# Kernel tuning notes

Measured on AMD Instinct MI355X. Metric: run time of the kernel, lower is better.

## Reference

```python
import jax, jax.numpy as jnp
import numpy as np

B, N, M, F, BF = 16, 1024, 12, 64, 128
N_CONV = 3
VOCAB = 100
BN_EPS = 1e-3  # keras BatchNormalization default epsilon


def _bn(x, gamma, beta):
    # inference-mode BN with moving_mean=0, moving_var=1 (keras defaults)
    return gamma * (x * (1.0 / jnp.sqrt(1.0 + BN_EPS))) + beta


def setup_inputs() -> dict:
    key = jax.random.key(0)
    ks = jax.random.split(key, 16)
    in_fea = 2 * F + BF
    inp = {
        'atom_types': jax.random.randint(ks[0], (B, N), 0, VOCAB, dtype=jnp.int32),
        'bond_fea': jax.random.normal(ks[1], (B, N, M, BF), dtype=jnp.float32),
        'nbr_list': jax.random.randint(ks[2], (B, N, M), 0, N, dtype=jnp.int32),
        'target_index': jax.random.randint(ks[3], (B, 64), 0, N, dtype=jnp.int32),
        'emb': jax.random.normal(ks[4], (VOCAB, F), dtype=jnp.float32) * 0.05,
        'core_w': jax.random.normal(ks[5], (N_CONV, in_fea, F), dtype=jnp.float32) / np.sqrt(in_fea),
        'core_b': jnp.zeros((N_CONV, F), dtype=jnp.float32),
        'filt_w': jax.random.normal(ks[6], (N_CONV, in_fea, 1), dtype=jnp.float32) / np.sqrt(in_fea),
        'filt_b': jnp.zeros((N_CONV, 1), dtype=jnp.float32),
        'bna_g': jnp.ones((N_CONV, F), dtype=jnp.float32),
        'bna_b': jnp.zeros((N_CONV, F), dtype=jnp.float32),
        'bnb_g': jnp.ones((N_CONV, F), dtype=jnp.float32),
        'bnb_b': jnp.zeros((N_CONV, F), dtype=jnp.float32),
        'dense_w': jax.random.normal(ks[7], (F, F), dtype=jnp.float32) / np.sqrt(F),
        'dense_b': jnp.zeros((F,), dtype=jnp.float32),
    }
    return inp


def _cgcnn_layer(x, bond_fea, nbr_list, cw, cb, fw, fb, bag, bab, bbg, bbb):
    # x: (B,N,F); bond_fea: (B,N,M,BF); nbr_list: (B,N,M)
    bidx = jnp.arange(x.shape[0])[:, None, None]
    atom_nbr = x[bidx, nbr_list]                       # (B,N,M,F) gather_nd
    atom_self = jnp.broadcast_to(x[:, :, None, :], atom_nbr.shape)
    total = jnp.concatenate([atom_self, atom_nbr, bond_fea], axis=-1)  # (B,N,M,2F+BF)
    core = total @ cw + cb                             # (B,N,M,F)
    filt = total @ fw + fb                             # (B,N,M,1)
    core = _bn(core, bag, bab)
    filt = jax.nn.softmax(filt, axis=2)                # softmax over neighbors
    core = jax.nn.relu(core)
    summed = jnp.mean(filt * core, axis=2)             # (B,N,F)
    summed = _bn(summed, bbg, bbb)
    return jax.nn.relu(x + summed)


def reference(atom_types, bond_fea, nbr_list, target_index, emb, core_w, core_b,
              filt_w, filt_b, bna_g, bna_b, bnb_g, bnb_b, dense_w, dense_b):
    x = emb[atom_types]                                # (B,N,F)
    for l in range(N_CONV):
        x = _cgcnn_layer(x, bond_fea, nbr_list, core_w[l], core_b[l],
                         filt_w[l], filt_b[l], bna_g[l], bna_b[l], bnb_g[l], bnb_b[l])
    bidx = jnp.arange(x.shape[0])[:, None]
    crys = x[bidx, target_index]                       # (B,N0,F) pooling gather
    crys = jax.nn.relu(crys)
    out = jax.nn.relu(crys @ dense_w + dense_b)        # (B,N0,F)
    return out
```

## Files before the change

### kernel.cpp

```cpp
#include <hip/hip_runtime.h>
#include <hip/hip_bf16.h>


#define BB 16
#define NN 1024
#define MM 12
#define FF 64
#define BFE 128
#define RT (BB * NN * MM)
#define S_BN 0.99950037f
#define WCOLS 208
#define WSTR 136

typedef __attribute__((ext_vector_type(8))) short bf16x8;
typedef __attribute__((ext_vector_type(4))) float f32x4;

static __device__ __forceinline__ unsigned short f2bf(float f) {
    union { float f; unsigned u; } c; c.f = f;
    unsigned r = c.u + 0x7fff + ((c.u >> 16) & 1);
    return (unsigned short)(r >> 16);
}
static __device__ __forceinline__ float bf2f(unsigned short s) {
    union { unsigned u; float f; } c; c.u = ((unsigned)s) << 16;
    return c.f;
}

__global__ void fold_w(const float* __restrict__ cw, const float* __restrict__ cb,
                       const float* __restrict__ g,  const float* __restrict__ bab,
                       float* __restrict__ cwp, float* __restrict__ cbp) {
    int i = blockIdx.x * 256 + threadIdx.x;
    if (i >= 3 * 256 * 64) return;
    int f = i & 63;
    int l = i / (256 * 64);
    float gs = g[l * 64 + f] * S_BN;
    cwp[i] = cw[i] * gs;
    if (((i >> 6) & 255) == 0)
        cbp[l * 64 + f] = cb[l * 64 + f] * gs + bab[l * 64 + f];
}

__global__ void prep_wT(const float* __restrict__ cw, const float* __restrict__ g,
                        const float* __restrict__ fw, unsigned short* __restrict__ wT) {
    int i = blockIdx.x * 256 + threadIdx.x;
    if (i >= WCOLS * WSTR) return;
    int col = i / WSTR, k = i % WSTR;
    float v = 0.f;
    if (k < 128) {
        if (col < 192) {
            int l = col >> 6, f = col & 63;
            v = cw[(l * 256 + 128 + k) * 64 + f] * g[l * 64 + f] * S_BN;
        } else if (col < 195) {
            int l = col - 192;
            v = fw[l * 256 + 128 + k];
        }
    }
    wT[i] = f2bf(v);
}

__global__ void embed_k(const int* __restrict__ at, const float* __restrict__ emb,
                        float* __restrict__ x) {
    int i = blockIdx.x * 256 + threadIdx.x;
    int f = i & 63;
    int bn = i >> 6;
    x[i] = emb[at[bn] * FF + f];
}

__global__ __launch_bounds__(256) void gemm_bond(
    const float* __restrict__ bond, const unsigned short* __restrict__ wT,
    unsigned short* __restrict__ core, float* __restrict__ filt) {
    __shared__ unsigned short bsh[WCOLS * WSTR];
    __shared__ unsigned short ash[64 * WSTR];
    int tid = threadIdx.x;
    int w = tid >> 6, lane = tid & 63;
    int row0 = blockIdx.x * 64;

    const float4* wsrc = (const float4*)wT;
    float4* wdst = (float4*)bsh;
    #pragma unroll
    for (int i = 0; i < 14; i++) {
        int idx = tid + 256 * i;
        if (idx < (WCOLS * WSTR * 2) / 16) wdst[idx] = wsrc[idx];
    }
    const float4* bsrc = (const float4*)(bond + (size_t)row0 * BFE);
    #pragma unroll
    for (int i = 0; i < 8; i++) {
        int idx = tid + 256 * i;
        float4 v = bsrc[idx];
        int r = idx >> 5, c4 = idx & 31;
        ushort4 h;
        h.x = f2bf(v.x); h.y = f2bf(v.y); h.z = f2bf(v.z); h.w = f2bf(v.w);
        *(ushort4*)&ash[r * WSTR + c4 * 4] = h;
    }
    __syncthreads();

    int m = lane & 15, quad = lane >> 4;
    f32x4 acc[13];
    #pragma unroll
    for (int t = 0; t < 13; t++) acc[t] = (f32x4){0.f, 0.f, 0.f, 0.f};

    #pragma unroll
    for (int c = 0; c < 4; c++) {
        bf16x8 af = *(const bf16x8*)&ash[(w * 16 + m) * WSTR + c * 32 + quad * 8];
        #pragma unroll
        for (int t = 0; t < 13; t++) {
            bf16x8 bfv = *(const bf16x8*)&bsh[(t * 16 + m) * WSTR + c * 32 + quad * 8];
            acc[t] = __builtin_amdgcn_mfma_f32_16x16x32_bf16(af, bfv, acc[t], 0, 0, 0);
        }
    }

    int rbase = row0 + w * 16 + quad * 4;
    #pragma unroll
    for (int t = 0; t < 12; t++) {
        int l = t >> 2;
        int f = (t & 3) * 16 + m;
        #pragma unroll
        for (int r = 0; r < 4; r++)
            core[((size_t)l * RT + rbase + r) * 64 + f] = f2bf(acc[t][r]);
    }
    if (m < 3) {
        #pragma unroll
        for (int r = 0; r < 4; r++)
            filt[(size_t)m * RT + rbase + r] = acc[12][r];
    }
}

__global__ __launch_bounds__(256) void atomproj(
    const float* __restrict__ x, const float* __restrict__ cwp_l,
    const float* __restrict__ cbp_l, const float* __restrict__ fw_l,
    const float* __restrict__ fb_l,
    float* __restrict__ ys, float* __restrict__ yn,
    float* __restrict__ fs, float* __restrict__ fn) {
    __shared__ float wsh[128 * 64];
    __shared__ float xs[4][64];
    int tid = threadIdx.x, w = tid >> 6, lane = tid & 63;
    #pragma unroll
    for (int i = 0; i < 8; i++)
        ((float4*)wsh)[tid + 256 * i] = ((const float4*)cwp_l)[tid + 256 * i];
    float fw1 = fw_l[lane], fw2 = fw_l[64 + lane];
    float cb = cbp_l[lane], fbv = fb_l[0];
    __syncthreads();
    #pragma unroll 1
    for (int it = 0; it < 4; it++) {
        int row = (blockIdx.x * 4 + it) * 4 + w;
        float xl = x[(size_t)row * 64 + lane];
        xs[w][lane] = xl;
        float a1 = cb, a2 = 0.f;
        #pragma unroll 16
        for (int k = 0; k < 64; k++) {
            float xv = xs[w][k];
            a1 += xv * wsh[k * 64 + lane];
            a2 += xv * wsh[(64 + k) * 64 + lane];
        }
        ys[(size_t)row * 64 + lane] = a1;
        yn[(size_t)row * 64 + lane] = a2;
        float p1 = xl * fw1, p2 = xl * fw2;
        #pragma unroll
        for (int off = 32; off; off >>= 1) {
            p1 += __shfl_xor(p1, off, 64);
            p2 += __shfl_xor(p2, off, 64);
        }
        if (lane == 0) { fs[row] = p1 + fbv; fn[row] = p2; }
    }
}

__global__ __launch_bounds__(256) void layer_ep(
    const float* __restrict__ x, const unsigned short* __restrict__ core_l,
    const float* __restrict__ filt_l, const int* __restrict__ nbr,
    const float* __restrict__ ys, const float* __restrict__ yn,
    const float* __restrict__ fs, const float* __restrict__ fn,
    const float* __restrict__ bbg, const float* __restrict__ bbb,
    float* __restrict__ xout) {
    int tid = threadIdx.x, w = tid >> 6, lane = tid & 63;
    int row = blockIdx.x * 4 + w;
    int base = (row >> 10) * NN;
    size_t rb = (size_t)row * MM;

    int jv[MM]; float fltv[MM], corev[MM];
    #pragma unroll
    for (int mm = 0; mm < MM; mm++) jv[mm] = nbr[rb + mm];
    float fsv = fs[row], ysv = ys[(size_t)row * 64 + lane];
    #pragma unroll
    for (int mm = 0; mm < MM; mm++)
        fltv[mm] = filt_l[rb + mm] + fsv + fn[base + jv[mm]];
    #pragma unroll
    for (int mm = 0; mm < MM; mm++)
        corev[mm] = bf2f(core_l[(rb + mm) * 64 + lane]) + ysv
                  + yn[(size_t)(base + jv[mm]) * 64 + lane];
    float fmax = -1e30f;
    #pragma unroll
    for (int mm = 0; mm < MM; mm++) fmax = fmaxf(fmax, fltv[mm]);
    float fsum = 0.f;
    #pragma unroll
    for (int mm = 0; mm < MM; mm++) { fltv[mm] = __expf(fltv[mm] - fmax); fsum += fltv[mm]; }
    float inv = 1.f / (12.f * fsum);
    float summed = 0.f;
    #pragma unroll
    for (int mm = 0; mm < MM; mm++) summed += fltv[mm] * fmaxf(corev[mm], 0.f);
    summed *= inv;
    float o = x[(size_t)row * 64 + lane] + bbg[lane] * (summed * S_BN) + bbb[lane];
    xout[(size_t)row * 64 + lane] = fmaxf(o, 0.f);
}

__global__ __launch_bounds__(256) void final_k(
    const float* __restrict__ x, const int* __restrict__ tidx,
    const float* __restrict__ dw, const float* __restrict__ db,
    float* __restrict__ out) {
    __shared__ float xs[4][64];
    __shared__ float wsh[64 * 64];
    int tid = threadIdx.x;
    int w = tid >> 6, lane = tid & 63;
    const float4* src = (const float4*)dw;
    float4* dst = (float4*)wsh;
    #pragma unroll
    for (int i = 0; i < 4; i++) dst[tid + 256 * i] = src[tid + 256 * i];
    int row = blockIdx.x * 4 + w;
    int b = row >> 6;
    int t = tidx[row];
    float xv = x[((size_t)b * NN + t) * 64 + lane];
    xs[w][lane] = fmaxf(xv, 0.f);
    __syncthreads();
    float a = db[lane];
    #pragma unroll 16
    for (int k = 0; k < 64; k++) a += xs[w][k] * wsh[k * 64 + lane];
    out[row * 64 + lane] = fmaxf(a, 0.f);
}

extern "C" void kernel_launch(void* const* d_in, const int* in_sizes, int n_in,
                              void* d_out, int out_size, void* d_ws, size_t ws_size,
                              hipStream_t stream) {
    const int*   at   = (const int*)d_in[0];
    const float* bond = (const float*)d_in[1];
    const int*   nbr  = (const int*)d_in[2];
    const int*   tgt  = (const int*)d_in[3];
    const float* emb  = (const float*)d_in[4];
    const float* cw   = (const float*)d_in[5];
    const float* cb   = (const float*)d_in[6];
    const float* fw   = (const float*)d_in[7];
    const float* fb   = (const float*)d_in[8];
    const float* bag  = (const float*)d_in[9];
    const float* bab  = (const float*)d_in[10];
    const float* bbg  = (const float*)d_in[11];
    const float* bbb  = (const float*)d_in[12];
    const float* dw   = (const float*)d_in[13];
    const float* db   = (const float*)d_in[14];

    float* ws   = (float*)d_ws;
    float* xA   = ws;
    float* xB   = xA + (size_t)BB * NN * FF;
    float* cwp  = xB + (size_t)BB * NN * FF;
    float* cbp  = cwp + 3 * 256 * 64;
    float* ys   = cbp + 192;
    float* yn   = ys + (size_t)BB * NN * FF;
    float* fs   = yn + (size_t)BB * NN * FF;
    float* fn   = fs + (size_t)BB * NN;
    float* filt = fn + (size_t)BB * NN;
    unsigned short* wT   = (unsigned short*)(filt + 3 * (size_t)RT);
    unsigned short* core = wT + WCOLS * WSTR;

    fold_w<<<(3 * 256 * 64 + 255) / 256, 256, 0, stream>>>(cw, cb, bag, bab, cwp, cbp);
    prep_wT<<<(WCOLS * WSTR + 255) / 256, 256, 0, stream>>>(cw, bag, fw, wT);
    embed_k<<<(BB * NN * FF) / 256, 256, 0, stream>>>(at, emb, xA);
    gemm_bond<<<RT / 64, 256, 0, stream>>>(bond, wT, core, filt);

    float* xin = xA;
    float* xout = xB;
    for (int l = 0; l < 3; l++) {
        atomproj<<<BB * NN / 16, 256, 0, stream>>>(
            xin, cwp + (size_t)l * 256 * 64, cbp + l * 64, fw + l * 256, fb + l,
            ys, yn, fs, fn);
        layer_ep<<<BB * NN / 4, 256, 0, stream>>>(
            xin, core + (size_t)l * RT * 64, filt + (size_t)l * RT, nbr,
            ys, yn, fs, fn, bbg + l * 64, bbb + l * 64, xout);
        float* t = xin; xin = xout; xout = t;
    }

    final_k<<<BB * 64 / 4, 256, 0, stream>>>(xin, tgt, dw, db, (float*)d_out);
}
```

Before: 290.3 us.

## Restructure bond GEMM: persistent blocks, register A-fragments, vectorized permuted stores

The bond-feature GEMM now runs on 512 blocks that each loop over three 128-row tiles, so the shared weight tile is loaded once per block instead of once per 64 rows. Each wave loads its A fragments straight from global memory into registers and converts them to bf16, removing the A staging buffer in shared memory. Each wave computes two 16-row fragments that share every B fragment it reads. Weight columns are permuted so every lane can write four contiguous bf16 outputs with one store. The cost is more accumulator registers, with occupancy capped at 2 blocks per CU by launch bounds, and uncoalesced strided global loads for A.

Result: slower. 348.1 us (+19.9%).

```diff
diff --git a/kernel.cpp b/kernel.cpp
--- a/kernel.cpp
+++ b/kernel.cpp
@@ -23,6 +23,14 @@
 static __device__ __forceinline__ float bf2f(unsigned short s) {
     union { unsigned u; float f; } c; c.u = ((unsigned)s) << 16;
     return c.f;
+}
+static __device__ __forceinline__ bf16x8 pack_bf16x8(float4 a, float4 b) {
+    union { unsigned u[4]; bf16x8 v; } r;
+    r.u[0] = (unsigned)f2bf(a.x) | ((unsigned)f2bf(a.y) << 16);
+    r.u[1] = (unsigned)f2bf(a.z) | ((unsigned)f2bf(a.w) << 16);
+    r.u[2] = (unsigned)f2bf(b.x) | ((unsigned)f2bf(b.y) << 16);
+    r.u[3] = (unsigned)f2bf(b.z) | ((unsigned)f2bf(b.w) << 16);
+    return r.v;
 }
 
 __global__ void fold_w(const float* __restrict__ cw, const float* __restrict__ cb,
@@ -46,7 +54,8 @@
     float v = 0.f;
     if (k < 128) {
         if (col < 192) {
-            int l = col >> 6, f = col & 63;
+            int l = col >> 6, p = col & 63;
+            int f = ((p & 15) << 2) | (p >> 4);
             v = cw[(l * 256 + 128 + k) * 64 + f] * g[l * 64 + f] * S_BN;
         } else if (col < 195) {
             int l = col - 192;
@@ -64,14 +73,35 @@
     x[i] = emb[at[bn] * FF + f];
 }
 
-__global__ __launch_bounds__(256) void gemm_bond(
+static __device__ __forceinline__ void store_tile(
+    const f32x4* acc, unsigned short* __restrict__ core,
+    float* __restrict__ filt, int crow, int m) {
+    #pragma unroll
+    for (int l = 0; l < 3; l++) {
+        #pragma unroll
+        for (int r = 0; r < 4; r++) {
+            ushort4 h;
+            h.x = f2bf(acc[l * 4 + 0][r]);
+            h.y = f2bf(acc[l * 4 + 1][r]);
+            h.z = f2bf(acc[l * 4 + 2][r]);
+            h.w = f2bf(acc[l * 4 + 3][r]);
+            *(ushort4*)&core[((size_t)l * RT + crow + r) * 64 + 4 * m] = h;
+        }
+    }
+    if (m < 3) {
+        #pragma unroll
+        for (int r = 0; r < 4; r++)
+            filt[(size_t)m * RT + crow + r] = acc[12][r];
+    }
+}
+
+__global__ __launch_bounds__(256, 2) void gemm_bond(
     const float* __restrict__ bond, const unsigned short* __restrict__ wT,
     unsigned short* __restrict__ core, float* __restrict__ filt) {
     __shared__ unsigned short bsh[WCOLS * WSTR];
-    __shared__ unsigned short ash[64 * WSTR];
     int tid = threadIdx.x;
     int w = tid >> 6, lane = tid & 63;
-    int row0 = blockIdx.x * 64;
+    int m = lane & 15, quad = lane >> 4;
 
     const float4* wsrc = (const float4*)wT;
     float4* wdst = (float4*)bsh;
@@ -80,46 +110,50 @@
         int idx = tid + 256 * i;
         if (idx < (WCOLS * WSTR * 2) / 16) wdst[idx] = wsrc[idx];
     }
-    const float4* bsrc = (const float4*)(bond + (size_t)row0 * BFE);
-    #pragma unroll
-    for (int i = 0; i < 8; i++) {
-        int idx = tid + 256 * i;
-        float4 v = bsrc[idx];
-        int r = idx >> 5, c4 = idx & 31;
-        ushort4 h;
-        h.x = f2bf(v.x); h.y = f2bf(v.y); h.z = f2bf(v.z); h.w = f2bf(v.w);
-        *(ushort4*)&ash[r * WSTR + c4 * 4] = h;
-    }
     __syncthreads();
 
-    int m = lane & 15, quad = lane >> 4;
-    f32x4 acc[13];
-    #pragma unroll
-    for (int t = 0; t < 13; t++) acc[t] = (f32x4){0.f, 0.f, 0.f, 0.f};
-
-    #pragma unroll
-    for (int c = 0; c < 4; c++) {
-        bf16x8 af = *(const bf16x8*)&ash[(w * 16 + m) * WSTR + c * 32 + quad * 8];
+    #pragma unroll 1
+    for (int it = 0; it < 3; it++) {
+        int row0 = blockIdx.x * 384 + it * 128;
+        const float* abase = bond + (size_t)(row0 + w * 32 + m) * BFE + quad * 8;
+
+        float4 areg[16];
+        #pragma unroll
+        for (int fr = 0; fr < 2; fr++) {
+            #pragma unroll
+            for (int c = 0; c < 4; c++) {
+                areg[fr * 8 + c * 2 + 0] = *(const float4*)(abase + fr * 16 * BFE + c * 32);
+                areg[fr * 8 + c * 2 + 1] = *(const float4*)(abase + fr * 16 * BFE + c * 32 + 4);
+            }
+        }
+        bf16x8 af[2][4];
+        #pragma unroll
+        for (int fr = 0; fr < 2; fr++)
+            #pragma unroll
+            for (int c = 0; c < 4; c++)
+                af[fr][c] = pack_bf16x8(areg[fr * 8 + c * 2], areg[fr * 8 + c * 2 + 1]);
+
+        f32x4 acc0[13], acc1[13];
         #pragma unroll
         for (int t = 0; t < 13; t++) {
-            bf16x8 bfv = *(const bf16x8*)&bsh[(t * 16 + m) * WSTR + c * 32 + quad * 8];
-            acc[t] = __builtin_amdgcn_mfma_f32_16x16x32_bf16(af, bfv, acc[t], 0, 0, 0);
-        }
-    }
-
-    int rbase = row0 + w * 16 + quad * 4;
-    #pragma unroll
-    for (int t = 0; t < 12; t++) {
-        int l = t >> 2;
-        int f = (t & 3) * 16 + m;
-        #pragma unroll
-        for (int r = 0; r < 4; r++)
-            core[((size_t)l * RT + rbase + r) * 64 + f] = f2bf(acc[t][r]);
-    }
-    if (m < 3) {
-        #pragma unroll
-        for (int r = 0; r < 4; r++)
-            filt[(size_t)m * RT + rbase + r] = acc[12][r];
+            acc0[t] = (f32x4){0.f, 0.f, 0.f, 0.f};
+            acc1[t] = (f32x4){0.f, 0.f, 0.f, 0.f};
+        }
+
+        #pragma unroll
+        for (int c = 0; c < 4; c++) {
+            bf16x8 a0 = af[0][c], a1 = af[1][c];
+            #pragma unroll
+            for (int t = 0; t < 13; t++) {
+                bf16x8 bfv = *(const bf16x8*)&bsh[(t * 16 + m) * WSTR + c * 32 + quad * 8];
+                acc0[t] = __builtin_amdgcn_mfma_f32_16x16x32_bf16(a0, bfv, acc0[t], 0, 0, 0);
+                acc1[t] = __builtin_amdgcn_mfma_f32_16x16x32_bf16(a1, bfv, acc1[t], 0, 0, 0);
+            }
+        }
+
+        int crow = row0 + w * 32 + quad * 4;
+        store_tile(acc0, core, filt, crow, m);
+        store_tile(acc1, core, filt, crow + 16, m);
     }
 }
 
@@ -259,7 +293,7 @@
     fold_w<<<(3 * 256 * 64 + 255) / 256, 256, 0, stream>>>(cw, cb, bag, bab, cwp, cbp);
     prep_wT<<<(WCOLS * WSTR + 255) / 256, 256, 0, stream>>>(cw, bag, fw, wT);
     embed_k<<<(BB * NN * FF) / 256, 256, 0, stream>>>(at, emb, xA);
-    gemm_bond<<<RT / 64, 256, 0, stream>>>(bond, wT, core, filt);
+    gemm_bond<<<512, 256, 0, stream>>>(bond, wT, core, filt);
 
     float* xin = xA;
     float* xout = xB;
```
